# Performance work log

Measured on AMD Instinct MI355X. Metric: run time of the kernel, lower is better.

## Reference

```python
import jax, jax.numpy as jnp
import numpy as np

B, N, C = 2, 2048, 1024
H = 16
D = C // H
HID = 4 * C
EPS = 1e-5


def layernorm(x, g, b):
    mu = jnp.mean(x, axis=-1, keepdims=True)
    var = jnp.var(x, axis=-1, keepdims=True)
    return (x - mu) * jax.lax.rsqrt(var + EPS) * g + b


def setup_inputs() -> dict:
    key = jax.random.key(0)
    ks = jax.random.split(key, 8)
    s = lambda fan_in: 1.0 / np.sqrt(fan_in)
    return {
        "x": jax.random.normal(ks[0], (B, N, C), dtype=jnp.float32),
        "ln1_g": jnp.ones((C,), jnp.float32),
        "ln1_b": jnp.zeros((C,), jnp.float32),
        "w_qkv": jax.random.normal(ks[1], (C, 3 * C), jnp.float32) * s(C),
        "w_proj": jax.random.normal(ks[2], (C, C), jnp.float32) * s(C),
        "b_proj": jnp.zeros((C,), jnp.float32),
        "ln2_g": jnp.ones((C,), jnp.float32),
        "ln2_b": jnp.zeros((C,), jnp.float32),
        "w_fc1": jax.random.normal(ks[3], (C, HID), jnp.float32) * s(C),
        "b_fc1": jnp.zeros((HID,), jnp.float32),
        "w_fc2": jax.random.normal(ks[4], (HID, C), jnp.float32) * s(HID),
        "b_fc2": jnp.zeros((C,), jnp.float32),
        "metadata": 0,
        "thw_shape": 2048,
    }


def reference(x, ln1_g, ln1_b, w_qkv, w_proj, b_proj, ln2_g, ln2_b,
              w_fc1, b_fc1, w_fc2, b_fc2, metadata, thw_shape):
    scale = 1.0 / np.sqrt(D)
    # --- attention branch (pre-norm) ---
    xn = layernorm(x, ln1_g, ln1_b)
    qkv = (xn @ w_qkv).reshape(B, N, 3, H, D)
    q = jnp.transpose(qkv[:, :, 0], (0, 2, 1, 3))  # [B,H,N,D]
    k = jnp.transpose(qkv[:, :, 1], (0, 2, 1, 3))
    v = jnp.transpose(qkv[:, :, 2], (0, 2, 1, 3))
    attn = jax.nn.softmax(jnp.einsum('bhnd,bhmd->bhnm', q, k) * scale, axis=-1)
    o = jnp.einsum('bhnm,bhmd->bhnd', attn, v)
    o = jnp.transpose(o, (0, 2, 1, 3)).reshape(B, N, C)
    x = x + (o @ w_proj + b_proj)
    # --- MLP branch (pre-norm) ---
    xn2 = layernorm(x, ln2_g, ln2_b)
    h = jax.nn.gelu(xn2 @ w_fc1 + b_fc1, approximate=False)  # torch GELU = exact erf
    x = x + (h @ w_fc2 + b_fc2)
    return x
```

## Files before the change

kernel.cpp:

```cpp
#include <hip/hip_runtime.h>

#define B_   2
#define N_   2048
#define C_   1024
#define H_   16
#define D_   64
#define HID_ 4096
#define M_   (B_ * N_)

typedef __attribute__((ext_vector_type(8))) short bf16x8;
typedef __attribute__((ext_vector_type(4))) float f32x4;

__device__ __forceinline__ unsigned short f2bf(float f) {
  unsigned int u = __builtin_bit_cast(unsigned int, f);
  u += 0x7fffu + ((u >> 16) & 1u);
  return (unsigned short)(u >> 16);
}

__device__ __forceinline__ unsigned int cvtpk(float a, float b) {
  unsigned int r;
  asm("v_cvt_pk_bf16_f32 %0, %1, %2" : "=v"(r) : "v"(a), "v"(b));
  return r;
}

__device__ __forceinline__ float exp2a(float x) {
  float r;
  asm("v_exp_f32 %0, %1" : "=v"(r) : "v"(x));
  return r;
}

__device__ __forceinline__ void gl2lds16(const void* g, void* l) {
  __builtin_amdgcn_global_load_lds(
      (const __attribute__((address_space(1))) unsigned int*)g,
      (__attribute__((address_space(3))) unsigned int*)l, 16, 0, 0);
}

#define LOG2E 1.44269504088896f

__global__ __launch_bounds__(256) void ln_kernel(const float* __restrict__ x,
                                                 const float* __restrict__ g,
                                                 const float* __restrict__ bta,
                                                 unsigned short* __restrict__ out) {
  int row  = blockIdx.x * 4 + (threadIdx.x >> 6);
  int lane = threadIdx.x & 63;
  const float* xr = x + (size_t)row * C_;
  float4 v[4];
  float s1 = 0.f, s2 = 0.f;
#pragma unroll
  for (int j = 0; j < 4; j++) {
    v[j] = *(const float4*)(xr + j * 256 + lane * 4);
    s1 += v[j].x + v[j].y + v[j].z + v[j].w;
    s2 += v[j].x * v[j].x + v[j].y * v[j].y + v[j].z * v[j].z + v[j].w * v[j].w;
  }
#pragma unroll
  for (int m = 1; m < 64; m <<= 1) { s1 += __shfl_xor(s1, m); s2 += __shfl_xor(s2, m); }
  float mu  = s1 * (1.0f / C_);
  float var = s2 * (1.0f / C_) - mu * mu;
  float rs  = rsqrtf(var + 1e-5f);
#pragma unroll
  for (int j = 0; j < 4; j++) {
    const float4 gv = *(const float4*)(g + j * 256 + lane * 4);
    const float4 bv = *(const float4*)(bta + j * 256 + lane * 4);
    ushort4 o;
    o.x = f2bf((v[j].x - mu) * rs * gv.x + bv.x);
    o.y = f2bf((v[j].y - mu) * rs * gv.y + bv.y);
    o.z = f2bf((v[j].z - mu) * rs * gv.z + bv.z);
    o.w = f2bf((v[j].w - mu) * rs * gv.w + bv.w);
    *(ushort4*)(out + (size_t)row * C_ + j * 256 + lane * 4) = o;
  }
}

__global__ __launch_bounds__(256) void wtrans_all(
    const float* __restrict__ w0, const float* __restrict__ w1,
    const float* __restrict__ w2, const float* __restrict__ w3,
    unsigned short* __restrict__ o0, unsigned short* __restrict__ o1,
    unsigned short* __restrict__ o2, unsigned short* __restrict__ o3) {
  int id = blockIdx.x;
  const float* W; unsigned short* Wt; int K, N, rel;
  if (id < 3072)      { W = w0; Wt = o0; K = 1024; N = 3072; rel = id; }
  else if (id < 4096) { W = w1; Wt = o1; K = 1024; N = 1024; rel = id - 3072; }
  else if (id < 8192) { W = w2; Wt = o2; K = 1024; N = 4096; rel = id - 4096; }
  else                { W = w3; Wt = o3; K = 4096; N = 1024; rel = id - 8192; }
  int nx = N >> 5;
  int n0 = (rel % nx) * 32, k0 = (rel / nx) * 32;
  __shared__ float t[32][33];
  int tx = threadIdx.x, ty = threadIdx.y;
#pragma unroll
  for (int j = 0; j < 4; j++)
    t[ty + j * 8][tx] = W[(size_t)(k0 + ty + j * 8) * N + n0 + tx];
  __syncthreads();
#pragma unroll
  for (int j = 0; j < 4; j++)
    Wt[(size_t)(n0 + ty + j * 8) * K + k0 + tx] = f2bf(t[tx][ty + j * 8]);
}

template <int MODE, int BN>
__global__ __launch_bounds__(256) void gemm_kernel(
    const unsigned short* __restrict__ A,
    const unsigned short* __restrict__ Wt,
    const float* __restrict__ bias,
    const float* __restrict__ resid,
    float* __restrict__ outf,
    unsigned short* __restrict__ outb0,
    int M, int N, int K) {
  constexpr int MT = (BN == 128) ? 4 : 2;
  __shared__ __align__(16) short As[128][64];
  __shared__ __align__(16) short Bs[BN][64];
  int tid = threadIdx.x;
  int w = tid >> 6, lane = tid & 63, r = lane & 15, quad = lane >> 4;
  int rowbase = (BN == 128) ? (w >> 1) * 64 : w * 32;
  int colbase = (BN == 128) ? (w & 1) * 64 : 0;

  int nwg = gridDim.x * gridDim.y;
  int lin = blockIdx.y * gridDim.x + blockIdx.x;
  if ((nwg & 7) == 0) {
    int cpx = nwg >> 3;
    lin = (lin & 7) * cpx + (lin >> 3);
  }
  int bx = lin % gridDim.x, by = lin / gridDim.x;
  int bM = by * 128, bN = bx * BN;

  int srow   = (w << 3) + (lane >> 3);
  int schunk = (lane & 7) ^ ((lane >> 3) & 7);
  const unsigned short* aP = A  + (size_t)(bM + srow) * K + schunk * 8;
  const unsigned short* bP = Wt + (size_t)(bN + srow) * K + schunk * 8;

  int pc0 = (quad ^ (r & 7)) * 8;

  f32x4 acc[MT][4];
#pragma unroll
  for (int i = 0; i < MT; i++)
#pragma unroll
    for (int j = 0; j < 4; j++) acc[i][j] = f32x4{0.f, 0.f, 0.f, 0.f};

  for (int k0 = 0; k0 < K; k0 += 64) {
    __syncthreads();
#pragma unroll
    for (int p = 0; p < 4; p++)
      gl2lds16(aP + (size_t)(p * 32) * K + k0, &As[p * 32 + (w << 3)][0]);
#pragma unroll
    for (int p = 0; p < BN / 32; p++)
      gl2lds16(bP + (size_t)(p * 32) * K + k0, &Bs[p * 32 + (w << 3)][0]);
    __syncthreads();
#pragma unroll
    for (int kh = 0; kh < 2; kh++) {
      int pc = pc0 ^ (kh * 32);
      bf16x8 af[MT], bfr[4];
#pragma unroll
      for (int mt = 0; mt < MT; mt++)
        af[mt] = *(const bf16x8*)&As[rowbase + mt * 16 + r][pc];
#pragma unroll
      for (int nt = 0; nt < 4; nt++)
        bfr[nt] = *(const bf16x8*)&Bs[colbase + nt * 16 + r][pc];
#pragma unroll
      for (int mt = 0; mt < MT; mt++)
#pragma unroll
        for (int nt = 0; nt < 4; nt++)
          acc[mt][nt] = __builtin_amdgcn_mfma_f32_16x16x32_bf16(af[mt], bfr[nt], acc[mt][nt], 0, 0, 0);
    }
  }

#pragma unroll
  for (int mt = 0; mt < MT; mt++) {
#pragma unroll
    for (int nt = 0; nt < 4; nt++) {
#pragma unroll
      for (int i = 0; i < 4; i++) {
        int gm = bM + rowbase + mt * 16 + quad * 4 + i;
        int gn = bN + colbase + nt * 16 + r;
        float val = acc[mt][nt][i];
        if (MODE == 1) {
          outf[(size_t)gm * N + gn] = val + bias[gn] + resid[(size_t)gm * N + gn];
        } else {
          float t = val + bias[gn];
          float gl = 0.5f * t * (1.0f + erff(t * 0.70710678118f));
          outb0[(size_t)gm * N + gn] = f2bf(gl);
        }
      }
    }
  }
}

template <int MODE>
__global__ __launch_bounds__(512, 2) void gemm256_kernel(
    const unsigned short* __restrict__ A,
    const unsigned short* __restrict__ Wt,
    const float* __restrict__ bias,
    unsigned short* __restrict__ outb0,
    unsigned short* __restrict__ outb1,
    unsigned short* __restrict__ outb2,
    int M, int N, int K) {
  __shared__ __align__(16) short As[2][256][64];
  __shared__ __align__(16) short Bs[2][256][64];
  const int tid = threadIdx.x;
  const int w = tid >> 6, lane = tid & 63, r = lane & 15, quad = lane >> 4;
  const int wr = w >> 2, wc = w & 3;
  const int bN = blockIdx.x * 256, bM = blockIdx.y * 256;

  const int srow   = (w << 3) + (lane >> 3);
  const int schunk = (lane & 7) ^ ((lane >> 3) & 7);
  const unsigned short* aSrc = A  + (size_t)(bM + srow) * K + schunk * 8;
  const unsigned short* bSrc = Wt + (size_t)(bN + srow) * K + schunk * 8;
  const int wrow = w << 3;

  const int ntiles = K >> 6;
  const int tmask  = ntiles - 1;

#define STAGE_H(t, h)                                                            \
  do {                                                                           \
    int b_ = (t) & 1, tt_ = (t) & tmask;                                         \
    if ((h) < 2) {                                                               \
      const unsigned short* p_ = aSrc + (size_t)((h) * 128) * K + tt_ * 64;      \
      gl2lds16(p_, &As[b_][(h) * 128 + wrow][0]);                                \
      gl2lds16(p_ + (size_t)64 * K, &As[b_][(h) * 128 + 64 + wrow][0]);          \
    } else {                                                                     \
      const unsigned short* p_ = bSrc + (size_t)(((h) - 2) * 128) * K + tt_ * 64;\
      gl2lds16(p_, &Bs[b_][((h) - 2) * 128 + wrow][0]);                          \
      gl2lds16(p_ + (size_t)64 * K, &Bs[b_][((h) - 2) * 128 + 64 + wrow][0]);    \
    }                                                                            \
  } while (0)

  f32x4 acc[8][4];
#pragma unroll
  for (int i = 0; i < 8; i++)
#pragma unroll
    for (int j = 0; j < 4; j++) acc[i][j] = f32x4{0.f, 0.f, 0.f, 0.f};

  bf16x8 af[4][2];
  bf16x8 bfr[4][2];

#define RD_A(b, msub)                                                            \
  {                                                                              \
    _Pragma("unroll") for (int mt_ = 0; mt_ < 4; mt_++)                          \
      _Pragma("unroll") for (int ks_ = 0; ks_ < 2; ks_++)                        \
        af[mt_][ks_] = *(const bf16x8*)&As[b][wr * 128 + (msub) * 64 + mt_ * 16 + r] \
                                          [((ks_ * 4 + quad) ^ (r & 7)) * 8];    \
  }
#define RD_B(b, nh)                                                              \
  {                                                                              \
    _Pragma("unroll") for (int nt_ = 0; nt_ < 2; nt_++)                          \
      _Pragma("unroll") for (int ks_ = 0; ks_ < 2; ks_++)                        \
        bfr[(nh) * 2 + nt_][ks_] =                                               \
            *(const bf16x8*)&Bs[b][wc * 64 + (nh) * 32 + nt_ * 16 + r]           \
                               [((ks_ * 4 + quad) ^ (r & 7)) * 8];               \
  }
#define MM_Q(msub, nh)                                                           \
  {                                                                              \
    _Pragma("unroll") for (int mt_ = 0; mt_ < 4; mt_++)                          \
      _Pragma("unroll") for (int nt_ = 0; nt_ < 2; nt_++)                        \
        _Pragma("unroll") for (int ks_ = 0; ks_ < 2; ks_++)                      \
          acc[(msub) * 4 + mt_][(nh) * 2 + nt_] =                                \
              __builtin_amdgcn_mfma_f32_16x16x32_bf16(                           \
                  af[mt_][ks_], bfr[(nh) * 2 + nt_][ks_],                        \
                  acc[(msub) * 4 + mt_][(nh) * 2 + nt_], 0, 0, 0);               \
  }

#define BARRIER() asm volatile("s_barrier" ::: "memory")
#define WAITL()   asm volatile("s_waitcnt lgkmcnt(0)" ::: "memory")
#define WAITV2()  asm volatile("s_waitcnt vmcnt(2)" ::: "memory")
#define PRIO1()   __builtin_amdgcn_s_setprio(1)
#define PRIO0()   __builtin_amdgcn_s_setprio(0)

  STAGE_H(0, 0); STAGE_H(0, 1); STAGE_H(0, 2); STAGE_H(0, 3);
  STAGE_H(1, 0);
  WAITV2();
  BARRIER();

  const int niter = ntiles >> 1;
  for (int i = 0; i < niter; i++) {
    const int tc = 2 * i;
    RD_A(0, 0); RD_B(0, 0);
    STAGE_H(tc + 1, 1);
    BARRIER(); WAITL();
    PRIO1(); MM_Q(0, 0); PRIO0();
    BARRIER();
    RD_B(0, 1);
    STAGE_H(tc + 1, 2);
    BARRIER(); WAITL();
    PRIO1(); MM_Q(0, 1); PRIO0();
    BARRIER();
    RD_A(0, 1);
    STAGE_H(tc + 1, 3);
    BARRIER(); WAITL();
    PRIO1(); MM_Q(1, 1); PRIO0();
    BARRIER();
    STAGE_H(tc + 2, 0);
    BARRIER(); WAITL();
    PRIO1(); MM_Q(1, 0); PRIO0();
    WAITV2();
    BARRIER();
    RD_A(1, 0); RD_B(1, 0);
    STAGE_H(tc + 2, 1);
    BARRIER(); WAITL();
    PRIO1(); MM_Q(0, 0); PRIO0();
    BARRIER();
    RD_B(1, 1);
    STAGE_H(tc + 2, 2);
    BARRIER(); WAITL();
    PRIO1(); MM_Q(0, 1); PRIO0();
    BARRIER();
    RD_A(1, 1);
    STAGE_H(tc + 2, 3);
    BARRIER(); WAITL();
    PRIO1(); MM_Q(1, 1); PRIO0();
    BARRIER();
    STAGE_H(tc + 3, 0);
    BARRIER(); WAITL();
    PRIO1(); MM_Q(1, 0); PRIO0();
    WAITV2();
    BARRIER();
  }

#pragma unroll
  for (int m = 0; m < 8; m++) {
#pragma unroll
    for (int n = 0; n < 4; n++) {
      int gm0 = bM + wr * 128 + m * 16 + quad * 4;
      int gn  = bN + wc * 64 + n * 16 + r;
      if (MODE == 0) {
        int s = gn >> 10, c = gn & 1023;
        int hh = c >> 6, d = c & 63;
        int b = gm0 >> 11, n0 = gm0 & 2047;
        if (s == 2) {
          unsigned int p0 = cvtpk(acc[m][n][0], acc[m][n][1]);
          unsigned int p1 = cvtpk(acc[m][n][2], acc[m][n][3]);
          *(uint2*)(outb2 + ((size_t)(b * H_ + hh) * D_ + d) * N_ + n0) = uint2{p0, p1};
        } else {
          unsigned short* dst = (s == 0) ? outb0 : outb1;
          float sc = (s == 0) ? 0.125f * LOG2E : 1.0f;
#pragma unroll
          for (int i2 = 0; i2 < 4; i2++) {
            size_t di = ((size_t)(b * H_ + hh) * N_ + n0 + i2) * D_ + d;
            dst[di] = f2bf(acc[m][n][i2] * sc);
          }
        }
      } else {
#pragma unroll
        for (int i2 = 0; i2 < 4; i2++) {
          float t = acc[m][n][i2] + bias[gn];
          float gl = 0.5f * t * (1.0f + erff(t * 0.70710678118f));
          outb0[(size_t)(gm0 + i2) * N + gn] = f2bf(gl);
        }
      }
    }
  }
#undef STAGE_H
#undef RD_A
#undef RD_B
#undef MM_Q
#undef BARRIER
#undef WAITL
#undef WAITV2
#undef PRIO1
#undef PRIO0
}

__global__ __launch_bounds__(512, 2) void attn_kernel(const unsigned short* __restrict__ qb,
                                                      const unsigned short* __restrict__ kb,
                                                      const unsigned short* __restrict__ vtb,
                                                      unsigned short* __restrict__ ob) {
  __shared__ __align__(16) short Ks[2][128][64];
  __shared__ __align__(16) short Vts[2][64][128];
  __shared__ __align__(16) short Pl[8 * 16 * 128];
  int tid = threadIdx.x;
  int w = tid >> 6, lane = tid & 63, r = lane & 15, quad = lane >> 4;
  int bh = blockIdx.x & 31, qt = blockIdx.x >> 5;
  const unsigned short* qh  = qb  + (size_t)bh * N_ * D_;
  const unsigned short* kh  = kb  + (size_t)bh * N_ * D_;
  const unsigned short* vth = vtb + (size_t)bh * D_ * N_;
  int swz = r & 7;

  bf16x8 qf[2][2];
#pragma unroll
  for (int mt = 0; mt < 2; mt++)
#pragma unroll
    for (int ks = 0; ks < 2; ks++)
      qf[mt][ks] = *(const bf16x8*)(qh + (size_t)(qt * 256 + w * 32 + mt * 16 + r) * D_ + ks * 32 + quad * 8);

  float mst[2] = {-1e30f, -1e30f}, lst[2] = {0.f, 0.f};
  f32x4 oacc[2][4];
#pragma unroll
  for (int mt = 0; mt < 2; mt++)
#pragma unroll
    for (int nt = 0; nt < 4; nt++) oacc[mt][nt] = f32x4{0.f, 0.f, 0.f, 0.f};

  const unsigned short* kBase = kh + (size_t)(tid >> 3) * D_ + ((tid & 7) ^ ((tid >> 3) & 7)) * 8;
  const unsigned short* vBase = vth + (size_t)(tid >> 4) * N_ + ((tid & 15) ^ ((tid >> 4) & 7)) * 8;

  short* Plw = &Pl[0] + w * 2048;

  gl2lds16(kBase,                        &Ks[0][(w << 3)][0]);
  gl2lds16(kBase + (size_t)64 * D_,      &Ks[0][64 + (w << 3)][0]);
  gl2lds16(vBase,                        &Vts[0][(w << 2)][0]);
  gl2lds16(vBase + (size_t)32 * N_,      &Vts[0][32 + (w << 2)][0]);
  __syncthreads();

  for (int t = 0; t < 16; t++) {
    const int cur = t & 1;
    if (t < 15) {
      const int nb = cur ^ 1;
      gl2lds16(kBase + (size_t)(t + 1) * 128 * D_,                  &Ks[nb][(w << 3)][0]);
      gl2lds16(kBase + (size_t)((t + 1) * 128 + 64) * D_,           &Ks[nb][64 + (w << 3)][0]);
      gl2lds16(vBase + (size_t)(t + 1) * 128,                       &Vts[nb][(w << 2)][0]);
      gl2lds16(vBase + (size_t)(t + 1) * 128 + (size_t)32 * N_,     &Vts[nb][32 + (w << 2)][0]);
    }

    f32x4 sacc[2][8];
#pragma unroll
    for (int mt = 0; mt < 2; mt++)
#pragma unroll
      for (int nt = 0; nt < 8; nt++) sacc[mt][nt] = f32x4{0.f, 0.f, 0.f, 0.f};
#pragma unroll
    for (int ks = 0; ks < 2; ks++) {
#pragma unroll
      for (int nt = 0; nt < 8; nt++) {
        bf16x8 kfr = *(const bf16x8*)&Ks[cur][nt * 16 + r][((ks * 4 + quad) ^ swz) * 8];
#pragma unroll
        for (int mt = 0; mt < 2; mt++)
          sacc[mt][nt] = __builtin_amdgcn_mfma_f32_16x16x32_bf16(kfr, qf[mt][ks], sacc[mt][nt], 0, 0, 0);
      }
    }

    bf16x8 vfr[4][4];
#pragma unroll
    for (int ks = 0; ks < 4; ks++)
#pragma unroll
      for (int nt2 = 0; nt2 < 4; nt2++)
        vfr[ks][nt2] = *(const bf16x8*)&Vts[cur][nt2 * 16 + r][((ks * 4 + quad) ^ swz) * 8];

#pragma unroll
    for (int mt = 0; mt < 2; mt++) {
      float tm = -1e30f;
#pragma unroll
      for (int nt = 0; nt < 8; nt++)
#pragma unroll
        for (int i = 0; i < 4; i++) tm = fmaxf(tm, sacc[mt][nt][i]);
      tm = fmaxf(tm, __shfl_xor(tm, 16));
      tm = fmaxf(tm, __shfl_xor(tm, 32));
      if (__ballot(tm > mst[mt] + 8.0f)) {
        float mnew = fmaxf(mst[mt], tm);
        float alpha = exp2a(mst[mt] - mnew);
        mst[mt] = mnew;
        lst[mt] *= alpha;
#pragma unroll
        for (int i = 0; i < 4; i++) {
          float av = __shfl(alpha, (lane & 48) | (quad * 4 + i));
#pragma unroll
          for (int nt2 = 0; nt2 < 4; nt2++) oacc[mt][nt2][i] *= av;
        }
      }
      float m = mst[mt];
      float rs = 0.f;
#pragma unroll
      for (int nt = 0; nt < 8; nt++)
#pragma unroll
        for (int i = 0; i < 4; i++) {
          float p = exp2a(sacc[mt][nt][i] - m);
          sacc[mt][nt][i] = p;
          rs += p;
        }
      rs += __shfl_xor(rs, 16);
      rs += __shfl_xor(rs, 32);
      lst[mt] += rs;
    }

#pragma unroll
    for (int mt = 0; mt < 2; mt++) {
#pragma unroll
      for (int nt = 0; nt < 8; nt++) {
        uint2 pw;
        pw.x = cvtpk(sacc[mt][nt][0], sacc[mt][nt][1]);
        pw.y = cvtpk(sacc[mt][nt][2], sacc[mt][nt][3]);
        *(uint2*)&Plw[r * 128 + (((nt * 2 + (quad >> 1)) ^ swz) * 8) + (quad & 1) * 4] = pw;
      }
      asm volatile("" ::: "memory");
#pragma unroll
      for (int ks = 0; ks < 4; ks++) {
        bf16x8 pfr = *(const bf16x8*)&Plw[r * 128 + ((ks * 4 + quad) ^ swz) * 8];
#pragma unroll
        for (int nt2 = 0; nt2 < 4; nt2++)
          oacc[mt][nt2] = __builtin_amdgcn_mfma_f32_16x16x32_bf16(pfr, vfr[ks][nt2], oacc[mt][nt2], 0, 0, 0);
      }
      asm volatile("" ::: "memory");
    }

    __syncthreads();
  }

  int bb = bh >> 4, hh = bh & 15;
#pragma unroll
  for (int mt = 0; mt < 2; mt++) {
#pragma unroll
    for (int i = 0; i < 4; i++) {
      float li = __shfl(lst[mt], (lane & 48) | (quad * 4 + i));
      float inv = 1.0f / li;
      int row = qt * 256 + w * 32 + mt * 16 + quad * 4 + i;
#pragma unroll
      for (int nt2 = 0; nt2 < 4; nt2++) {
        int d = nt2 * 16 + r;
        ob[((size_t)bb * N_ + row) * C_ + hh * D_ + d] = f2bf(oacc[mt][nt2][i] * inv);
      }
    }
  }
}

extern "C" void kernel_launch(void* const* d_in, const int* in_sizes, int n_in,
                              void* d_out, int out_size, void* d_ws, size_t ws_size,
                              hipStream_t stream) {
  const float* x     = (const float*)d_in[0];
  const float* ln1g  = (const float*)d_in[1];
  const float* ln1b  = (const float*)d_in[2];
  const float* wqkv  = (const float*)d_in[3];
  const float* wproj = (const float*)d_in[4];
  const float* bproj = (const float*)d_in[5];
  const float* ln2g  = (const float*)d_in[6];
  const float* ln2b  = (const float*)d_in[7];
  const float* wfc1  = (const float*)d_in[8];
  const float* bfc1  = (const float*)d_in[9];
  const float* wfc2  = (const float*)d_in[10];
  const float* bfc2  = (const float*)d_in[11];
  float* out = (float*)d_out;

  const size_t MB = 1u << 20;
  if (ws_size < 88 * MB) return;
  char* w = (char*)d_ws;
  unsigned short* xn    = (unsigned short*)(w + 0 * MB);
  unsigned short* qbuf  = (unsigned short*)(w + 8 * MB);
  unsigned short* kbuf  = (unsigned short*)(w + 16 * MB);
  unsigned short* hbuf  = (unsigned short*)(w + 0 * MB);
  unsigned short* obuf  = (unsigned short*)(w + 32 * MB);
  float*          x2    = (float*)         (w + 40 * MB);
  unsigned short* xn2   = (unsigned short*)(w + 56 * MB);
  unsigned short* vtb   = (unsigned short*)(w + 56 * MB);
  unsigned short* wqkvt = (unsigned short*)(w + 64 * MB);
  unsigned short* wprjt = (unsigned short*)(w + 70 * MB);
  unsigned short* wfc1t = (unsigned short*)(w + 72 * MB);
  unsigned short* wfc2t = (unsigned short*)(w + 80 * MB);

  ln_kernel<<<M_ / 4, 256, 0, stream>>>(x, ln1g, ln1b, xn);
  wtrans_all<<<12288, dim3(32, 8), 0, stream>>>(wqkv, wproj, wfc1, wfc2,
                                                wqkvt, wprjt, wfc1t, wfc2t);

  gemm256_kernel<0><<<dim3(3 * C_ / 256, M_ / 256), 512, 0, stream>>>(
      xn, wqkvt, nullptr, qbuf, kbuf, vtb, M_, 3 * C_, C_);
  attn_kernel<<<B_ * H_ * (N_ / 256), 512, 0, stream>>>(qbuf, kbuf, vtb, obuf);
  gemm_kernel<1, 128><<<dim3(C_ / 128, M_ / 128), 256, 0, stream>>>(
      obuf, wprjt, bproj, x, x2, nullptr, M_, C_, C_);
  ln_kernel<<<M_ / 4, 256, 0, stream>>>(x2, ln2g, ln2b, xn2);
  gemm256_kernel<2><<<dim3(HID_ / 256, M_ / 256), 512, 0, stream>>>(
      xn2, wfc1t, bfc1, hbuf, nullptr, nullptr, M_, HID_, C_);
  gemm_kernel<1, 128><<<dim3(C_ / 128, M_ / 128), 256, 0, stream>>>(
      hbuf, wfc2t, bfc2, x2, out, nullptr, M_, C_, HID_);
}
```

Measured before the change: 372.3 us.

## Double-buffer projection GEMMs with 128x64 tiles and swizzle block order in 256 GEMM

Replaces the single-buffered 128x128 GEMM used for the attention projection and FC2 with a double-buffered 128x64 kernel that prefetches the next K tile into a second LDS buffer while computing the current one. This removes one barrier per iteration and hides global-to-LDS latency, and the smaller N tile doubles the number of workgroups (512 instead of 256) to fill more CUs. It also applies the XCD-aware block-index remapping to the 256x256 GEMM. In exchange, each workgroup reuses less data per loaded A tile, and LDS use per block rises.

```diff
diff --git a/kernel.cpp b/kernel.cpp
--- a/kernel.cpp
+++ b/kernel.cpp
@@ -94,31 +94,25 @@
     Wt[(size_t)(n0 + ty + j * 8) * K + k0 + tx] = f2bf(t[tx][ty + j * 8]);
 }
 
-template <int MODE, int BN>
-__global__ __launch_bounds__(256) void gemm_kernel(
+__global__ __launch_bounds__(256) void gemm_db_kernel(
     const unsigned short* __restrict__ A,
     const unsigned short* __restrict__ Wt,
     const float* __restrict__ bias,
     const float* __restrict__ resid,
     float* __restrict__ outf,
-    unsigned short* __restrict__ outb0,
     int M, int N, int K) {
-  constexpr int MT = (BN == 128) ? 4 : 2;
-  __shared__ __align__(16) short As[128][64];
-  __shared__ __align__(16) short Bs[BN][64];
+  __shared__ __align__(16) short As[2][128][64];
+  __shared__ __align__(16) short Bs[2][64][64];
   int tid = threadIdx.x;
   int w = tid >> 6, lane = tid & 63, r = lane & 15, quad = lane >> 4;
-  int rowbase = (BN == 128) ? (w >> 1) * 64 : w * 32;
-  int colbase = (BN == 128) ? (w & 1) * 64 : 0;
+  int rowbase = w * 32;
 
   int nwg = gridDim.x * gridDim.y;
   int lin = blockIdx.y * gridDim.x + blockIdx.x;
-  if ((nwg & 7) == 0) {
-    int cpx = nwg >> 3;
-    lin = (lin & 7) * cpx + (lin >> 3);
-  }
+  int cpx = nwg >> 3;
+  lin = (lin & 7) * cpx + (lin >> 3);
   int bx = lin % gridDim.x, by = lin / gridDim.x;
-  int bM = by * 128, bN = bx * BN;
+  int bM = by * 128, bN = bx * 64;
 
   int srow   = (w << 3) + (lane >> 3);
   int schunk = (lane & 7) ^ ((lane >> 3) & 7);
@@ -127,58 +121,60 @@
 
   int pc0 = (quad ^ (r & 7)) * 8;
 
-  f32x4 acc[MT][4];
-#pragma unroll
-  for (int i = 0; i < MT; i++)
+  f32x4 acc[2][4];
+#pragma unroll
+  for (int i = 0; i < 2; i++)
 #pragma unroll
     for (int j = 0; j < 4; j++) acc[i][j] = f32x4{0.f, 0.f, 0.f, 0.f};
 
-  for (int k0 = 0; k0 < K; k0 += 64) {
-    __syncthreads();
-#pragma unroll
-    for (int p = 0; p < 4; p++)
-      gl2lds16(aP + (size_t)(p * 32) * K + k0, &As[p * 32 + (w << 3)][0]);
-#pragma unroll
-    for (int p = 0; p < BN / 32; p++)
-      gl2lds16(bP + (size_t)(p * 32) * K + k0, &Bs[p * 32 + (w << 3)][0]);
-    __syncthreads();
+#define STAGE_DB(kt, b)                                                       \
+  do {                                                                        \
+    int k0_ = (kt) * 64;                                                      \
+    _Pragma("unroll") for (int p = 0; p < 4; p++)                             \
+      gl2lds16(aP + (size_t)(p * 32) * K + k0_, &As[b][p * 32 + (w << 3)][0]);\
+    _Pragma("unroll") for (int p = 0; p < 2; p++)                             \
+      gl2lds16(bP + (size_t)(p * 32) * K + k0_, &Bs[b][p * 32 + (w << 3)][0]);\
+  } while (0)
+
+  const int nk = K >> 6;
+  STAGE_DB(0, 0);
+  __syncthreads();
+
+  for (int kt = 0; kt < nk; kt++) {
+    const int cb = kt & 1;
+    if (kt + 1 < nk) STAGE_DB(kt + 1, cb ^ 1);
 #pragma unroll
     for (int kh = 0; kh < 2; kh++) {
       int pc = pc0 ^ (kh * 32);
-      bf16x8 af[MT], bfr[4];
-#pragma unroll
-      for (int mt = 0; mt < MT; mt++)
-        af[mt] = *(const bf16x8*)&As[rowbase + mt * 16 + r][pc];
+      bf16x8 af[2], bfr[4];
+#pragma unroll
+      for (int mt = 0; mt < 2; mt++)
+        af[mt] = *(const bf16x8*)&As[cb][rowbase + mt * 16 + r][pc];
 #pragma unroll
       for (int nt = 0; nt < 4; nt++)
-        bfr[nt] = *(const bf16x8*)&Bs[colbase + nt * 16 + r][pc];
-#pragma unroll
-      for (int mt = 0; mt < MT; mt++)
+        bfr[nt] = *(const bf16x8*)&Bs[cb][nt * 16 + r][pc];
+#pragma unroll
+      for (int mt = 0; mt < 2; mt++)
 #pragma unroll
         for (int nt = 0; nt < 4; nt++)
           acc[mt][nt] = __builtin_amdgcn_mfma_f32_16x16x32_bf16(af[mt], bfr[nt], acc[mt][nt], 0, 0, 0);
     }
-  }
-
-#pragma unroll
-  for (int mt = 0; mt < MT; mt++) {
+    __syncthreads();
+  }
+
+#pragma unroll
+  for (int mt = 0; mt < 2; mt++) {
 #pragma unroll
     for (int nt = 0; nt < 4; nt++) {
 #pragma unroll
       for (int i = 0; i < 4; i++) {
         int gm = bM + rowbase + mt * 16 + quad * 4 + i;
-        int gn = bN + colbase + nt * 16 + r;
-        float val = acc[mt][nt][i];
-        if (MODE == 1) {
-          outf[(size_t)gm * N + gn] = val + bias[gn] + resid[(size_t)gm * N + gn];
-        } else {
-          float t = val + bias[gn];
-          float gl = 0.5f * t * (1.0f + erff(t * 0.70710678118f));
-          outb0[(size_t)gm * N + gn] = f2bf(gl);
-        }
-      }
-    }
-  }
+        int gn = bN + nt * 16 + r;
+        outf[(size_t)gm * N + gn] = acc[mt][nt][i] + bias[gn] + resid[(size_t)gm * N + gn];
+      }
+    }
+  }
+#undef STAGE_DB
 }
 
 template <int MODE>
@@ -195,7 +191,12 @@
   const int tid = threadIdx.x;
   const int w = tid >> 6, lane = tid & 63, r = lane & 15, quad = lane >> 4;
   const int wr = w >> 2, wc = w & 3;
-  const int bN = blockIdx.x * 256, bM = blockIdx.y * 256;
+
+  int nwg = gridDim.x * gridDim.y;
+  int lin = blockIdx.y * gridDim.x + blockIdx.x;
+  int cpx = nwg >> 3;
+  lin = (lin & 7) * cpx + (lin >> 3);
+  const int bN = (lin % gridDim.x) * 256, bM = (lin / gridDim.x) * 256;
 
   const int srow   = (w << 3) + (lane >> 3);
   const int schunk = (lane & 7) ^ ((lane >> 3) & 7);
@@ -544,11 +545,11 @@
   gemm256_kernel<0><<<dim3(3 * C_ / 256, M_ / 256), 512, 0, stream>>>(
       xn, wqkvt, nullptr, qbuf, kbuf, vtb, M_, 3 * C_, C_);
   attn_kernel<<<B_ * H_ * (N_ / 256), 512, 0, stream>>>(qbuf, kbuf, vtb, obuf);
-  gemm_kernel<1, 128><<<dim3(C_ / 128, M_ / 128), 256, 0, stream>>>(
-      obuf, wprjt, bproj, x, x2, nullptr, M_, C_, C_);
+  gemm_db_kernel<<<dim3(C_ / 64, M_ / 128), 256, 0, stream>>>(
+      obuf, wprjt, bproj, x, x2, M_, C_, C_);
   ln_kernel<<<M_ / 4, 256, 0, stream>>>(x2, ln2g, ln2b, xn2);
   gemm256_kernel<2><<<dim3(HID_ / 256, M_ / 256), 512, 0, stream>>>(
       xn2, wfc1t, bfc1, hbuf, nullptr, nullptr, M_, HID_, C_);
-  gemm_kernel<1, 128><<<dim3(C_ / 128, M_ / 128), 256, 0, stream>>>(
-      hbuf, wfc2t, bfc2, x2, out, nullptr, M_, C_, HID_);
-}
+  gemm_db_kernel<<<dim3(C_ / 64, M_ / 128), 256, 0, stream>>>(
+      hbuf, wfc2t, bfc2, x2, out, M_, C_, HID_);
+}
```

Result: faster. 342.5 us (-8.0%).
